# Optimization experiments

Hardware: AMD Instinct MI355X
Metric: run time of the kernel (lower is better)

Reference implementation:

```python
import jax, jax.numpy as jnp
import numpy as np
import math

D_MODEL = 512
N_HEADS = 16
HEAD_DIM = D_MODEL // N_HEADS  # 32
ROPE_BASE = 10000.0
B, T = 2, 2048


def build_rope_cache(seq_len, dim, base):
    inv_freq = 1.0 / (base ** (jnp.arange(0, dim, 2, dtype=jnp.float32) / dim))  # (dim/2,)
    t = jnp.arange(seq_len, dtype=jnp.float32)
    freqs = jnp.outer(t, inv_freq)                  # (T, dim/2)
    emb = jnp.concatenate([freqs, freqs], axis=-1)  # (T, dim)
    return jnp.cos(emb), jnp.sin(emb)


def rotate_half(x):
    x1, x2 = jnp.split(x, 2, axis=-1)
    return jnp.concatenate([-x2, x1], axis=-1)


def apply_rope(x, cos, sin):
    # x: (B,H,T,hd); cos/sin: (T,hd) broadcast over B,H
    return x * cos + rotate_half(x) * sin


def setup_inputs() -> dict:
    key = jax.random.key(0)
    k1, k2, k3 = jax.random.split(key, 3)
    x = jax.random.normal(k1, (B, T, D_MODEL), dtype=jnp.float32)
    w_qkv = jax.random.normal(k2, (3 * D_MODEL, D_MODEL), dtype=jnp.float32) * 0.02
    w_o = jax.random.normal(k3, (D_MODEL, D_MODEL), dtype=jnp.float32) * 0.02
    return {"x": x, "w_qkv": w_qkv, "w_o": w_o}


def reference(x, w_qkv, w_o):
    Bx, Tx, C = x.shape
    H, hd = N_HEADS, HEAD_DIM
    qkv = x @ w_qkv.T                                   # (B,T,3C)
    qkv = qkv.reshape(Bx, Tx, 3, H, hd).transpose(0, 2, 3, 1, 4)  # (B,3,H,T,hd)
    q, k, v = qkv[:, 0], qkv[:, 1], qkv[:, 2]
    cos, sin = build_rope_cache(Tx, hd, ROPE_BASE)
    q = apply_rope(q, cos, sin)
    k = apply_rope(k, cos, sin)
    scale = 1.0 / math.sqrt(hd)
    scores = jnp.einsum('bhqd,bhkd->bhqk', q, k) * scale  # (B,H,T,T)
    causal = jnp.tril(jnp.ones((Tx, Tx), dtype=bool))
    scores = jnp.where(causal, scores, jnp.finfo(scores.dtype).min)
    attn = jax.nn.softmax(scores, axis=-1)
    out = jnp.einsum('bhqk,bhkd->bhqd', attn, v)          # (B,H,T,hd)
    out = out.transpose(0, 2, 1, 3).reshape(Bx, Tx, C)    # (B,T,C)
    return out @ w_o.T
```

## Files before the change

kernel.cpp:

```cpp
#include <hip/hip_runtime.h>
#include <hip/hip_bf16.h>
#include <math.h>

#define D_MODEL 512
#define N_HEADS 16
#define HEAD_DIM 32
#define T_SEQ 2048
#define B_SZ 2
#define NTOK (B_SZ * T_SEQ)
#define QKV_DIM (3 * D_MODEL)

typedef short short8 __attribute__((ext_vector_type(8)));
typedef float f32x4  __attribute__((ext_vector_type(4)));

__device__ __forceinline__ float bf2f(unsigned int u16) {
    union { unsigned int i; float f; } v;
    v.i = u16 << 16;
    return v.f;
}

__device__ __forceinline__ unsigned short f2bf(float f) {
    union { float f; unsigned int i; } v;
    v.f = f;
    unsigned int lsb = (v.i >> 16) & 1u;
    v.i += 0x7fffu + lsb;
    return (unsigned short)(v.i >> 16);
}

__device__ __forceinline__ unsigned short f2bf_trunc(float f) {
    union { float f; unsigned int i; } v;
    v.f = f;
    return (unsigned short)(v.i >> 16);
}

__device__ __forceinline__ void gld_lds16(const void* g, void* l) {
    __builtin_amdgcn_global_load_lds(
        (const __attribute__((address_space(1))) void*)g,
        (__attribute__((address_space(3))) void*)l, 16, 0, 0);
}

#define N4_X   (NTOK * D_MODEL / 4)
#define N4_WQ  (QKV_DIM * D_MODEL / 4)
#define N4_WO  (D_MODEL * D_MODEL / 4)
__global__ __launch_bounds__(256) void cvt_all(const float* __restrict__ x,
                                               const float* __restrict__ wq,
                                               const float* __restrict__ wo,
                                               unsigned short* __restrict__ xb,
                                               unsigned short* __restrict__ wqb,
                                               unsigned short* __restrict__ wob) {
    int i = blockIdx.x * 256 + threadIdx.x;
    const float* in;
    unsigned short* out;
    int k;
    if (i < N4_X)                { in = x;  out = xb;  k = i; }
    else if (i < N4_X + N4_WQ)   { in = wq; out = wqb; k = i - N4_X; }
    else if (i < N4_X + N4_WQ + N4_WO) { in = wo; out = wob; k = i - N4_X - N4_WQ; }
    else return;
    float4 v = ((const float4*)in)[k];
    ushort4 o;
    o.x = f2bf(v.x); o.y = f2bf(v.y); o.z = f2bf(v.z); o.w = f2bf(v.w);
    ((ushort4*)out)[k] = o;
}

#define LOG2_10000_D16 0.8304820237218405f
#define QSCALE_LOG2 0.2550348788f

template<int MT, int LDA, int LDC, bool OUT_BF16, bool ROPE>
__global__ __launch_bounds__(256) void gemm_nt(const unsigned short* __restrict__ A,
                                               const unsigned short* __restrict__ B,
                                               void* __restrict__ Cout,
                                               unsigned short* __restrict__ kb,
                                               unsigned short* __restrict__ vt) {
    __shared__ unsigned short Als[MT * 64];
    __shared__ unsigned short Bls[64 * 64];

    const int tid = threadIdx.x;
    const int m0 = blockIdx.y * MT;
    const int n0 = blockIdx.x * 64;

    const int wid  = tid >> 6;
    const int lane = tid & 63;
    const int c    = lane & 15;
    const int quad = lane >> 4;
    const int wm = (wid >> 1) * (MT / 2);
    const int wn = (wid & 1) * 32;
    const int MI = MT / 32;

    f32x4 acc[MI][2];
#pragma unroll
    for (int i = 0; i < MI; ++i)
#pragma unroll
        for (int j = 0; j < 2; ++j) acc[i][j] = (f32x4)0.f;

    const int srow = wid * 8 + (lane >> 3);
    const int schk = lane & 7;

    for (int k0 = 0; k0 < 512; k0 += 64) {
#pragma unroll
        for (int it = 0; it < MT / 32; ++it) {
            const unsigned short* g = A + (size_t)(m0 + it * 32 + srow) * LDA + k0 + schk * 8;
            gld_lds16(g, &Als[(it * 32 + srow) * 64 + schk * 8]);
        }
#pragma unroll
        for (int it = 0; it < 2; ++it) {
            const unsigned short* g = B + (size_t)(n0 + it * 32 + srow) * 512 + k0 + schk * 8;
            gld_lds16(g, &Bls[(it * 32 + srow) * 64 + schk * 8]);
        }
        __syncthreads();

#pragma unroll
        for (int kk = 0; kk < 2; ++kk) {
            short8 af[MI], bfr[2];
#pragma unroll
            for (int i = 0; i < MI; ++i)
                af[i] = *(const short8*)&Als[(wm + i * 16 + c) * 64 + kk * 32 + quad * 8];
#pragma unroll
            for (int j = 0; j < 2; ++j)
                bfr[j] = *(const short8*)&Bls[(wn + j * 16 + c) * 64 + kk * 32 + quad * 8];
#pragma unroll
            for (int i = 0; i < MI; ++i)
#pragma unroll
                for (int j = 0; j < 2; ++j)
                    acc[i][j] = __builtin_amdgcn_mfma_f32_16x16x32_bf16(af[i], bfr[j], acc[i][j], 0, 0, 0);
        }
        __syncthreads();
    }

    if (ROPE) {
        const int sec = n0 >> 9;
        if (sec == 0) {
            const float invf = exp2f(-LOG2_10000_D16 * (float)c);
#pragma unroll
            for (int i = 0; i < MI; ++i)
#pragma unroll
                for (int r = 0; r < 4; ++r) {
                    int t = (m0 + wm + i * 16 + quad * 4 + r) & (T_SEQ - 1);
                    float ss, cc;
                    sincosf((float)t * invf, &ss, &cc);
                    float e0 = acc[i][0][r], e1 = acc[i][1][r];
                    acc[i][0][r] = (e0 * cc - e1 * ss) * QSCALE_LOG2;
                    acc[i][1][r] = (e1 * cc + e0 * ss) * QSCALE_LOG2;
                }
        } else if (sec == 1) {
            const float invf = exp2f(-LOG2_10000_D16 * (float)c);
            const int head = ((n0 - 512) + wn) >> 5;
#pragma unroll
            for (int i = 0; i < MI; ++i)
#pragma unroll
                for (int r = 0; r < 4; ++r) {
                    int mm = m0 + wm + i * 16 + quad * 4 + r;
                    int t = mm & (T_SEQ - 1);
                    float ss, cc;
                    sincosf((float)t * invf, &ss, &cc);
                    float e0 = acc[i][0][r], e1 = acc[i][1][r];
                    float k0v = e0 * cc - e1 * ss;
                    float k1v = e1 * cc + e0 * ss;
                    int bh = (mm >> 11) * 16 + head;
                    int s = (t & 3) ^ ((t >> 2) & 3);
                    unsigned short* row = kb + ((size_t)(bh * 2048 + t)) * 32;
                    row[((((c) >> 3) ^ s) << 3) + (c & 7)]        = f2bf(k0v);
                    row[((((16 + c) >> 3) ^ s) << 3) + (c & 7)]   = f2bf(k1v);
                }
            return;
        } else {
#pragma unroll
            for (int i = 0; i < MI; ++i)
#pragma unroll
                for (int j = 0; j < 2; ++j) {
                    int nl = n0 - 1024 + wn + j * 16;
                    int head = nl >> 5;
                    int d = (nl & 16) + c;
                    int mm = m0 + wm + i * 16 + quad * 4;
                    int bI = mm >> 11;
                    int pos = mm & (T_SEQ - 1);
                    int phys = ((pos >> 3) & 7) ^ (d & 7);
                    size_t base = ((size_t)((bI * 16 + head) * 32 + d)) * 2048
                                  + (pos & ~63) + (phys << 3) + (pos & 7);
                    ushort4 st;
                    st.x = f2bf(acc[i][j][0]); st.y = f2bf(acc[i][j][1]);
                    st.z = f2bf(acc[i][j][2]); st.w = f2bf(acc[i][j][3]);
                    *(ushort4*)(vt + base) = st;
                }
            return;
        }
    }

    if (OUT_BF16) {
        unsigned short* Cb = (unsigned short*)Cout;
#pragma unroll
        for (int i = 0; i < MI; ++i)
#pragma unroll
            for (int j = 0; j < 2; ++j)
#pragma unroll
                for (int r = 0; r < 4; ++r) {
                    int mm = m0 + wm + i * 16 + quad * 4 + r;
                    int nn = n0 + wn + j * 16 + c;
                    Cb[(size_t)mm * LDC + nn] = f2bf(acc[i][j][r]);
                }
    } else {
        float* Cf = (float*)Cout;
#pragma unroll
        for (int i = 0; i < MI; ++i)
#pragma unroll
            for (int j = 0; j < 2; ++j)
#pragma unroll
                for (int r = 0; r < 4; ++r) {
                    int mm = m0 + wm + i * 16 + quad * 4 + r;
                    int nn = n0 + wn + j * 16 + c;
                    Cf[(size_t)mm * LDC + nn] = acc[i][j][r];
                }
    }
}

__global__ __launch_bounds__(256) void flash_attn(unsigned short* __restrict__ qb,
                                                  const unsigned short* __restrict__ kb,
                                                  const unsigned short* __restrict__ vt) {
    __shared__ unsigned short KtL[64 * 32];
    __shared__ unsigned short VtL[32 * 64];
    __shared__ unsigned short Pl[4 * 16 * 64];

    const int idx   = blockIdx.x;
    const int qtile = 31 - (idx >> 5);
    const int bh    = idx & 31;
    const int b = bh >> 4, h = bh & 15;
    const int tid  = threadIdx.x;
    const int wid  = tid >> 6;
    const int lane = tid & 63;
    const int c    = lane & 15;
    const int quad = lane >> 4;

    const int q0w = qtile * 64 + wid * 16;
    const int sK = (c & 3) ^ ((c >> 2) & 3);
    const int sP = c & 7;

    short8 qf = *(const short8*)(qb + ((size_t)(b * T_SEQ + q0w + c)) * 512 + h * HEAD_DIM + quad * 8);

    f32x4 accO[2];
    accO[0] = (f32x4)0.f; accO[1] = (f32x4)0.f;
    float l_r[4] = {0.f, 0.f, 0.f, 0.f};

    unsigned short* plw = &Pl[wid * 16 * 64];

    const int krow = tid >> 2, kch = tid & 3;
    const int vd   = tid >> 3, vch = tid & 7;
    const unsigned short* kbase = kb + (size_t)bh * 2048 * 32 + (size_t)krow * 32 + kch * 8;
    const unsigned short* vbase = vt + ((size_t)(bh * 32 + vd)) * 2048 + vch * 8;

    uint4 kreg = *(const uint4*)(kbase);
    uint4 vreg = *(const uint4*)(vbase);

    const int nkt = qtile + 1;
    for (int kt = 0; kt < nkt; ++kt) {
        __syncthreads();
        *(uint4*)&KtL[tid * 8] = kreg;
        *(uint4*)&VtL[tid * 8] = vreg;
        __syncthreads();

        if (kt + 1 < nkt) {
            kreg = *(const uint4*)(kbase + (size_t)(kt + 1) * 64 * 32);
            vreg = *(const uint4*)(vbase + (kt + 1) * 64);
        }

        f32x4 sv[4];
#pragma unroll
        for (int j = 0; j < 4; ++j) {
            short8 kf = *(const short8*)&KtL[(j * 16 + c) * 32 + ((quad ^ sK) << 3)];
            f32x4 z = (f32x4)0.f;
            sv[j] = __builtin_amdgcn_mfma_f32_16x16x32_bf16(qf, kf, z, 0, 0, 0);
        }

        if (kt == qtile) {
#pragma unroll
            for (int j = 0; j < 4; ++j)
#pragma unroll
                for (int r = 0; r < 4; ++r)
                    if (j * 16 + c > wid * 16 + quad * 4 + r) sv[j][r] = -30000.f;
        }

#pragma unroll
        for (int j = 0; j < 4; ++j)
#pragma unroll
            for (int r = 0; r < 4; ++r) {
                float p = exp2f(sv[j][r]);
                l_r[r] += p;
                int row = quad * 4 + r;
                plw[row * 64 + (((j * 2 + (c >> 3)) ^ (row & 7)) << 3) + (c & 7)] = f2bf_trunc(p);
            }

#pragma unroll
        for (int kk = 0; kk < 2; ++kk) {
            short8 pf = *(const short8*)&plw[c * 64 + (((kk * 4 + quad) ^ sP) << 3)];
#pragma unroll
            for (int ns = 0; ns < 2; ++ns) {
                short8 vf = *(const short8*)&VtL[(ns * 16 + c) * 64 + (((kk * 4 + quad) ^ sP) << 3)];
                accO[ns] = __builtin_amdgcn_mfma_f32_16x16x32_bf16(pf, vf, accO[ns], 0, 0, 0);
            }
        }
    }

#pragma unroll
    for (int r = 0; r < 4; ++r) {
        float lr = l_r[r];
        lr += __shfl_xor(lr, 1);
        lr += __shfl_xor(lr, 2);
        lr += __shfl_xor(lr, 4);
        lr += __shfl_xor(lr, 8);
        float inv = 1.f / lr;
        int qg = q0w + quad * 4 + r;
        unsigned short* op = qb + ((size_t)(b * T_SEQ + qg)) * 512 + h * HEAD_DIM;
#pragma unroll
        for (int ns = 0; ns < 2; ++ns)
            op[ns * 16 + c] = f2bf(accO[ns][r] * inv);
    }
}

extern "C" void kernel_launch(void* const* d_in, const int* in_sizes, int n_in,
                              void* d_out, int out_size, void* d_ws, size_t ws_size,
                              hipStream_t stream) {
    const float* x     = (const float*)d_in[0];
    const float* w_qkv = (const float*)d_in[1];
    const float* w_o   = (const float*)d_in[2];
    float* out = (float*)d_out;

    unsigned short* qb  = (unsigned short*)d_ws;
    unsigned short* kb  = qb  + (size_t)NTOK * D_MODEL;
    unsigned short* vt  = kb  + (size_t)32 * 2048 * 32;
    unsigned short* xb  = vt  + (size_t)32 * 32 * 2048;
    unsigned short* wqb = xb  + (size_t)NTOK * D_MODEL;
    unsigned short* wob = wqb + (size_t)QKV_DIM * D_MODEL;

    {
        int total = N4_X + N4_WQ + N4_WO;
        cvt_all<<<(total + 255) / 256, 256, 0, stream>>>(x, w_qkv, w_o, xb, wqb, wob);
    }
    {
        dim3 grid(QKV_DIM / 64, NTOK / 128);
        gemm_nt<128, D_MODEL, D_MODEL, true, true><<<grid, 256, 0, stream>>>(xb, wqb, qb, kb, vt);
    }
    {
        flash_attn<<<1024, 256, 0, stream>>>(qb, kb, vt);
    }
    {
        dim3 grid(D_MODEL / 64, NTOK / 64);
        gemm_nt<64, D_MODEL, D_MODEL, false, false><<<grid, 256, 0, stream>>>(qb, wob, out, nullptr, nullptr);
    }
}
```

Measured before the change: 121.6 us.

## Double-buffer K/V tiles in flash attention and precompute RoPE table

The flash attention loop now keeps two LDS buffers for K and V. The next tile is stored into the spare buffer after the current tile's MFMAs, so each iteration needs one barrier instead of two. MFMA sections are wrapped in s_setprio to favour matrix issue. Separately, the RoPE cos/sin values are computed once per (t, dim) into a table by the conversion kernel and read by the QKV GEMM epilogue, replacing per-element sincosf; this costs extra LDS, an extra table in the workspace, and global loads in the epilogue.

After: 124.1 us. +2.1%, slower.

```diff
diff --git a/kernel.cpp b/kernel.cpp
--- a/kernel.cpp
+++ b/kernel.cpp
@@ -9,6 +9,10 @@
 #define B_SZ 2
 #define NTOK (B_SZ * T_SEQ)
 #define QKV_DIM (3 * D_MODEL)
+
+#define LOG2_10000_D16 0.8304820237218405f
+#define QSCALE_LOG2 0.2550348788f
+#define NROPE (T_SEQ * 16)
 
 typedef short short8 __attribute__((ext_vector_type(8)));
 typedef float f32x4  __attribute__((ext_vector_type(4)));
@@ -47,30 +51,39 @@
                                                const float* __restrict__ wo,
                                                unsigned short* __restrict__ xb,
                                                unsigned short* __restrict__ wqb,
-                                               unsigned short* __restrict__ wob) {
+                                               unsigned short* __restrict__ wob,
+                                               float2* __restrict__ rope) {
     int i = blockIdx.x * 256 + threadIdx.x;
+    if (i >= N4_X + N4_WQ + N4_WO) {
+        int kk = i - (N4_X + N4_WQ + N4_WO);
+        if (kk < NROPE) {
+            int t = kk >> 4, cd = kk & 15;
+            float invf = exp2f(-LOG2_10000_D16 * (float)cd);
+            float ss, cc;
+            sincosf((float)t * invf, &ss, &cc);
+            rope[kk] = make_float2(cc, ss);
+        }
+        return;
+    }
     const float* in;
     unsigned short* out;
     int k;
     if (i < N4_X)                { in = x;  out = xb;  k = i; }
     else if (i < N4_X + N4_WQ)   { in = wq; out = wqb; k = i - N4_X; }
-    else if (i < N4_X + N4_WQ + N4_WO) { in = wo; out = wob; k = i - N4_X - N4_WQ; }
-    else return;
+    else                         { in = wo; out = wob; k = i - N4_X - N4_WQ; }
     float4 v = ((const float4*)in)[k];
     ushort4 o;
     o.x = f2bf(v.x); o.y = f2bf(v.y); o.z = f2bf(v.z); o.w = f2bf(v.w);
     ((ushort4*)out)[k] = o;
 }
-
-#define LOG2_10000_D16 0.8304820237218405f
-#define QSCALE_LOG2 0.2550348788f
 
 template<int MT, int LDA, int LDC, bool OUT_BF16, bool ROPE>
 __global__ __launch_bounds__(256) void gemm_nt(const unsigned short* __restrict__ A,
                                                const unsigned short* __restrict__ B,
                                                void* __restrict__ Cout,
                                                unsigned short* __restrict__ kb,
-                                               unsigned short* __restrict__ vt) {
+                                               unsigned short* __restrict__ vt,
+                                               const float2* __restrict__ rope) {
     __shared__ unsigned short Als[MT * 64];
     __shared__ unsigned short Bls[64 * 64];
 
@@ -129,20 +142,19 @@
     if (ROPE) {
         const int sec = n0 >> 9;
         if (sec == 0) {
-            const float invf = exp2f(-LOG2_10000_D16 * (float)c);
+            const float2* rp = rope + c;
 #pragma unroll
             for (int i = 0; i < MI; ++i)
 #pragma unroll
                 for (int r = 0; r < 4; ++r) {
                     int t = (m0 + wm + i * 16 + quad * 4 + r) & (T_SEQ - 1);
-                    float ss, cc;
-                    sincosf((float)t * invf, &ss, &cc);
+                    float2 cs = rp[t * 16];
                     float e0 = acc[i][0][r], e1 = acc[i][1][r];
-                    acc[i][0][r] = (e0 * cc - e1 * ss) * QSCALE_LOG2;
-                    acc[i][1][r] = (e1 * cc + e0 * ss) * QSCALE_LOG2;
+                    acc[i][0][r] = (e0 * cs.x - e1 * cs.y) * QSCALE_LOG2;
+                    acc[i][1][r] = (e1 * cs.x + e0 * cs.y) * QSCALE_LOG2;
                 }
         } else if (sec == 1) {
-            const float invf = exp2f(-LOG2_10000_D16 * (float)c);
+            const float2* rp = rope + c;
             const int head = ((n0 - 512) + wn) >> 5;
 #pragma unroll
             for (int i = 0; i < MI; ++i)
@@ -150,11 +162,10 @@
                 for (int r = 0; r < 4; ++r) {
                     int mm = m0 + wm + i * 16 + quad * 4 + r;
                     int t = mm & (T_SEQ - 1);
-                    float ss, cc;
-                    sincosf((float)t * invf, &ss, &cc);
+                    float2 cs = rp[t * 16];
                     float e0 = acc[i][0][r], e1 = acc[i][1][r];
-                    float k0v = e0 * cc - e1 * ss;
-                    float k1v = e1 * cc + e0 * ss;
+                    float k0v = e0 * cs.x - e1 * cs.y;
+                    float k1v = e1 * cs.x + e0 * cs.y;
                     int bh = (mm >> 11) * 16 + head;
                     int s = (t & 3) ^ ((t >> 2) & 3);
                     unsigned short* row = kb + ((size_t)(bh * 2048 + t)) * 32;
@@ -215,8 +226,8 @@
 __global__ __launch_bounds__(256) void flash_attn(unsigned short* __restrict__ qb,
                                                   const unsigned short* __restrict__ kb,
                                                   const unsigned short* __restrict__ vt) {
-    __shared__ unsigned short KtL[64 * 32];
-    __shared__ unsigned short VtL[32 * 64];
+    __shared__ unsigned short KtL[2][64 * 32];
+    __shared__ unsigned short VtL[2][32 * 64];
     __shared__ unsigned short Pl[4 * 16 * 64];
 
     const int idx   = blockIdx.x;
@@ -248,26 +259,28 @@
 
     uint4 kreg = *(const uint4*)(kbase);
     uint4 vreg = *(const uint4*)(vbase);
+    *(uint4*)&KtL[0][tid * 8] = kreg;
+    *(uint4*)&VtL[0][tid * 8] = vreg;
+    __syncthreads();
 
     const int nkt = qtile + 1;
     for (int kt = 0; kt < nkt; ++kt) {
-        __syncthreads();
-        *(uint4*)&KtL[tid * 8] = kreg;
-        *(uint4*)&VtL[tid * 8] = vreg;
-        __syncthreads();
-
-        if (kt + 1 < nkt) {
+        const int cur = kt & 1;
+        const bool pf_next = (kt + 1 < nkt);
+        if (pf_next) {
             kreg = *(const uint4*)(kbase + (size_t)(kt + 1) * 64 * 32);
-            vreg = *(const uint4*)(vbase + (kt + 1) * 64);
+            vreg = *(const uint4*)(vbase + (size_t)(kt + 1) * 64);
         }
 
         f32x4 sv[4];
+        __builtin_amdgcn_s_setprio(1);
 #pragma unroll
         for (int j = 0; j < 4; ++j) {
-            short8 kf = *(const short8*)&KtL[(j * 16 + c) * 32 + ((quad ^ sK) << 3)];
+            short8 kf = *(const short8*)&KtL[cur][(j * 16 + c) * 32 + ((quad ^ sK) << 3)];
             f32x4 z = (f32x4)0.f;
             sv[j] = __builtin_amdgcn_mfma_f32_16x16x32_bf16(qf, kf, z, 0, 0, 0);
         }
+        __builtin_amdgcn_s_setprio(0);
 
         if (kt == qtile) {
 #pragma unroll
@@ -287,15 +300,23 @@
                 plw[row * 64 + (((j * 2 + (c >> 3)) ^ (row & 7)) << 3) + (c & 7)] = f2bf_trunc(p);
             }
 
+        __builtin_amdgcn_s_setprio(1);
 #pragma unroll
         for (int kk = 0; kk < 2; ++kk) {
             short8 pf = *(const short8*)&plw[c * 64 + (((kk * 4 + quad) ^ sP) << 3)];
 #pragma unroll
             for (int ns = 0; ns < 2; ++ns) {
-                short8 vf = *(const short8*)&VtL[(ns * 16 + c) * 64 + (((kk * 4 + quad) ^ sP) << 3)];
+                short8 vf = *(const short8*)&VtL[cur][(ns * 16 + c) * 64 + (((kk * 4 + quad) ^ sP) << 3)];
                 accO[ns] = __builtin_amdgcn_mfma_f32_16x16x32_bf16(pf, vf, accO[ns], 0, 0, 0);
             }
         }
+        __builtin_amdgcn_s_setprio(0);
+
+        if (pf_next) {
+            *(uint4*)&KtL[cur ^ 1][tid * 8] = kreg;
+            *(uint4*)&VtL[cur ^ 1][tid * 8] = vreg;
+        }
+        __syncthreads();
     }
 
 #pragma unroll
@@ -328,20 +349,21 @@
     unsigned short* xb  = vt  + (size_t)32 * 32 * 2048;
     unsigned short* wqb = xb  + (size_t)NTOK * D_MODEL;
     unsigned short* wob = wqb + (size_t)QKV_DIM * D_MODEL;
+    float2*         rope = (float2*)(wob + (size_t)D_MODEL * D_MODEL);
 
     {
-        int total = N4_X + N4_WQ + N4_WO;
-        cvt_all<<<(total + 255) / 256, 256, 0, stream>>>(x, w_qkv, w_o, xb, wqb, wob);
+        int total = N4_X + N4_WQ + N4_WO + NROPE;
+        cvt_all<<<(total + 255) / 256, 256, 0, stream>>>(x, w_qkv, w_o, xb, wqb, wob, rope);
     }
     {
         dim3 grid(QKV_DIM / 64, NTOK / 128);
-        gemm_nt<128, D_MODEL, D_MODEL, true, true><<<grid, 256, 0, stream>>>(xb, wqb, qb, kb, vt);
+        gemm_nt<128, D_MODEL, D_MODEL, true, true><<<grid, 256, 0, stream>>>(xb, wqb, qb, kb, vt, rope);
     }
     {
         flash_attn<<<1024, 256, 0, stream>>>(qb, kb, vt);
     }
     {
         dim3 grid(D_MODEL / 64, NTOK / 64);
-        gemm_nt<64, D_MODEL, D_MODEL, false, false><<<grid, 256, 0, stream>>>(qb, wob, out, nullptr, nullptr);
-    }
-}
+        gemm_nt<64, D_MODEL, D_MODEL, false, false><<<grid, 256, 0, stream>>>(qb, wob, out, nullptr, nullptr, nullptr);
+    }
+}
```
